# Kernel optimization log

Hardware: AMD Instinct MI355X
Metric: run time of the kernel (lower is better)

Reference implementation:

```python
import jax, jax.numpy as jnp
import numpy as np

B, N, NB, E, H, A, K, D = 32, 512, 10, 1024, 256, 82, 4, 3


def setup_inputs() -> dict:
    key = jax.random.key(0)
    ks = iter(jax.random.split(key, 64))
    f = lambda shape: jax.random.normal(next(ks), shape, jnp.float32) * 0.05
    inp = {
        "atom_fea": jax.random.normal(next(ks), (B, N, A), jnp.float32),
        "bond_fea": jax.random.normal(next(ks), (B, E, 6), jnp.float32),
        "d_anb": jax.random.randint(next(ks), (B, N, NB), 0, N),
        "d_bnb": jax.random.randint(next(ks), (B, N, NB), 0, E),
        "d_nbs_mask": (jax.random.uniform(next(ks), (B, N, NB)) < 0.8).astype(jnp.float32),
        "d_mask": (jax.random.uniform(next(ks), (B, N)) < 0.9).astype(jnp.float32),
        "Wv": f((A, H)), "bv": f((H,)),
        "Wa_main": f((D, K, H, H)), "ba_main": f((D, K, H)),
        "Wa_super": f((D, K, H, H)), "ba_super": f((D, K, H)),
        "Wm": f((D, K, H, H)), "bm": f((D, K, H)),
        "Wbmm": f((D, K, H)), "bbmm": f((D, K)),
        "Wm2s": f((D, K * H, H)), "bm2s": f((D, H)),
        "Ws2m": f((D, H, H)), "bs2m": f((D, H)),
        "Wsup": f((D, H, H)), "bsup": f((D, H)),
        "Wzm1": f((D, H, H)), "bzm1": f((D, H)),
        "Wzm2": f((D, H, H)), "bzm2": f((D, H)),
        "Wzs1": f((D, H, H)), "bzs1": f((D, H)),
        "Wzs2": f((D, H, H)), "bzs2": f((D, H)),
        "Wu2": f((D, H + 6, H)), "bu2": f((D, H)),
        "Wu1": f((D, 2 * H, H)), "bu1": f((D, H)),
    }
    return inp


def mask_softmax(a, mask):
    a_max = jnp.max(a, -1, keepdims=True)
    e = jnp.exp(a - a_max) * mask
    return e / (jnp.sum(e, -1, keepdims=True) + 1e-6)


def _forward(atom_fea, bond_fea, d_nbs_mask, d_mask,
             Wv, bv, Wa_main, ba_main, Wa_super, ba_super, Wm, bm, Wbmm, bbmm,
             Wm2s, bm2s, Ws2m, bs2m, Wsup, bsup,
             Wzm1, bzm1, Wzm2, bzm2, Wzs1, bzs1, Wzs2, bzs2,
             Wu2, bu2, Wu1, bu1, d_anb, d_bnb):
    Bn = atom_fea.shape[0]
    bidx = jnp.arange(Bn)[:, None, None]
    # vertex embedding (default leaky_relu slope 0.01)
    vf = jax.nn.leaky_relu(atom_fea @ Wv + bv, 0.01)            # [B,N,H]
    sf = jnp.sum(vf * d_mask[:, :, None], axis=1, keepdims=True)  # [B,1,H]
    mask3 = d_nbs_mask[..., None]                               # [B,N,NB,1]
    for d in range(D):
        # --- multi-head main->super attention (vectorized over heads k) ---
        a_main = jnp.tanh(jnp.einsum('bnh,khj->bknj', vf, Wa_main[d]) + ba_main[d][None, :, None, :])
        a_super = jnp.tanh(jnp.einsum('boh,khj->bkoj', sf, Wa_super[d]) + ba_super[d][None, :, None, :])
        a = jnp.einsum('bknh,kh->bkn', a_main * a_super, Wbmm[d]) + bbmm[d][None, :, None]
        attn = mask_softmax(a, d_mask[:, None, :])               # [B,K,N]
        mvf = jnp.einsum('bnh,khj->bknj', vf, Wm[d]) + bm[d][None, :, None, :]
        m2s = jnp.einsum('bkn,bknh->bkh', attn, mvf).reshape(Bn, 1, K * H)
        main_to_super = jnp.tanh(m2s @ Wm2s[d] + bm2s[d])        # [B,1,H]
        # --- wln unit: gather neighbors, MLP, masked sum (slope 0.1) ---
        vnei = vf[bidx, d_anb]                                   # [B,N,NB,H]
        enei = bond_fea[bidx, d_bnb]                             # [B,N,NB,6]
        lnei = jnp.concatenate([vnei, enei], -1)                 # [B,N,NB,H+6]
        nei = jax.nn.leaky_relu(lnei @ Wu2[d] + bu2[d], 0.1)
        nei = jnp.sum(nei * mask3, axis=2)                       # [B,N,H]
        main_self = jax.nn.leaky_relu(jnp.concatenate([vf, nei], -1) @ Wu1[d] + bu1[d], 0.1)
        # --- GRU-style gated updates ---
        super_to_main = jnp.tanh(sf @ Ws2m[d] + bs2m[d])         # [B,1,H]
        super_self = jnp.tanh(sf @ Wsup[d] + bsup[d])            # [B,1,H]
        z_main = jax.nn.sigmoid(main_self @ Wzm1[d] + bzm1[d] + super_to_main @ Wzm2[d] + bzm2[d])
        vf = (1 - z_main) * main_self + z_main * super_to_main
        z_sup = jax.nn.sigmoid(super_self @ Wzs1[d] + bzs1[d] + main_to_super @ Wzs2[d] + bzs2[d])
        sf = (1 - z_sup) * super_self + z_sup * main_to_super    # [B,1,H]; sum over dim 1 is a no-op
    return vf, sf


def reference(atom_fea, bond_fea, d_anb, d_bnb, d_nbs_mask, d_mask,
              Wv, bv, Wa_main, ba_main, Wa_super, ba_super, Wm, bm, Wbmm, bbmm,
              Wm2s, bm2s, Ws2m, bs2m, Wsup, bsup,
              Wzm1, bzm1, Wzm2, bzm2, Wzs1, bzs1, Wzs2, bzs2,
              Wu2, bu2, Wu1, bu1):
    return _forward(atom_fea, bond_fea, d_nbs_mask, d_mask,
                    Wv, bv, Wa_main, ba_main, Wa_super, ba_super, Wm, bm, Wbmm, bbmm,
                    Wm2s, bm2s, Ws2m, bs2m, Wsup, bsup,
                    Wzm1, bzm1, Wzm2, bzm2, Wzs1, bzs1, Wzs2, bzs2,
                    Wu2, bu2, Wu1, bu1, d_anb, d_bnb)
```

## Files before the change

### kernel.cpp

```cpp
#include <hip/hip_runtime.h>
#include <hip/hip_bf16.h>

#define B_ 32
#define N_ 512
#define NB_ 10
#define E_ 1024
#define H_ 256
#define A_ 82
#define K_ 4
#define D_ 3
#define M_ (B_*N_)

typedef unsigned short u16;
typedef __attribute__((ext_vector_type(8))) short bf16x8;
typedef __attribute__((ext_vector_type(4))) float f32x4;

__device__ __forceinline__ float b2f(u16 u){
    unsigned int x = ((unsigned int)u) << 16;
    return __builtin_bit_cast(float, x);
}
__device__ __forceinline__ u16 f2b(float f){
    unsigned int x = __builtin_bit_cast(unsigned int, f);
    unsigned int lsb = (x >> 16) & 1u;
    x += 0x7fffu + lsb;
    return (u16)(x >> 16);
}
__device__ __forceinline__ float sigmoidf_(float x){ return 1.f/(1.f+expf(-x)); }

static constexpr int CVT_N[31] = {
    B_*E_*6, B_*N_*NB_, B_*N_,
    A_*H_, H_,
    D_*K_*H_*H_, D_*K_*H_, D_*K_*H_*H_, D_*K_*H_,
    D_*K_*H_*H_, D_*K_*H_, D_*K_*H_, D_*K_,
    D_*K_*H_*H_, D_*H_, D_*H_*H_, D_*H_,
    D_*H_*H_, D_*H_, D_*H_*H_, D_*H_,
    D_*H_*H_, D_*H_, D_*H_*H_, D_*H_,
    D_*H_*H_, D_*H_, D_*(H_+6)*H_, D_*H_,
    D_*2*H_*H_, D_*H_
};
struct Offs { long v[32]; };
static constexpr Offs mk_offs(){
    Offs o{}; o.v[0]=0;
    for(int i=0;i<31;i++) o.v[i+1]=o.v[i]+CVT_N[i];
    return o;
}
static constexpr Offs CVT_OFF = mk_offs();

struct Ptrs { const void* p[31]; };

__global__ void k_detect(const unsigned short* __restrict__ wv_raw, int* __restrict__ flag){
    float v = b2f(wv_raw[threadIdx.x]);
    bool plaus = (v==v) && (fabsf(v) < 100.0f);
    unsigned long long m = __ballot(plaus);
    if (threadIdx.x==0) *flag = (m == ~0ULL) ? 1 : 0;
}

__global__ void k_cvt(Ptrs ptrs, float* __restrict__ dst, const int* __restrict__ flag){
    long i4 = (long)blockIdx.x*256 + threadIdx.x;
    const long TOT4 = CVT_OFF.v[31]/4;
    if (i4 >= TOT4) return;
    long e = i4*4;
    int t = 0;
    #pragma unroll
    for(int i=1;i<31;i++) t += (e >= CVT_OFF.v[i]) ? 1 : 0;
    long l4 = i4 - CVT_OFF.v[t]/4;
    const void* src = ptrs.p[t];
    float4 o;
    if (*flag){
        ushort4 u = ((const ushort4*)src)[l4];
        o.x=b2f(u.x); o.y=b2f(u.y); o.z=b2f(u.z); o.w=b2f(u.w);
    } else {
        o = ((const float4*)src)[l4];
    }
    *(float4*)(dst + CVT_OFF.v[t] + l4*4) = o;
}

__global__ void k_wt(const float* __restrict__ Wam, const float* __restrict__ Wu2,
                     const float* __restrict__ Wu1, const float* __restrict__ Wzm1,
                     u16* __restrict__ WT){
    int mi = blockIdx.z;
    const float* src;
    if (mi<12)      src = Wam  + (size_t)mi*H_*H_;
    else if (mi<15) src = Wu2  + (size_t)(mi-12)*(H_+6)*H_;
    else if (mi<18) src = Wu1  + (size_t)(mi-15)*2*H_*H_;
    else if (mi<21) src = Wu1  + (size_t)(mi-18)*2*H_*H_ + (size_t)H_*H_;
    else            src = Wzm1 + (size_t)(mi-21)*H_*H_;
    __shared__ float t[32][33];
    int x = threadIdx.x, y = threadIdx.y;
    int k0 = blockIdx.y*32, n0 = blockIdx.x*32;
    for(int yy=y; yy<32; yy+=8) t[yy][x] = src[(size_t)(k0+yy)*H_ + n0+x];
    __syncthreads();
    u16* dst = WT + ((size_t)mi*8 + (k0>>5))*8192;
    int quad = x>>3, j = x&7;
    for(int yy=y; yy<32; yy+=8){
        int n = n0+yy, nt = n>>4, lv = n&15;
        dst[nt*512 + quad*128 + lv*8 + j] = f2b(t[x][yy]);
    }
}

__global__ void k_embed(const u16* __restrict__ atom, const float* __restrict__ Wv,
                        const float* __restrict__ bv, float* __restrict__ vf,
                        u16* __restrict__ vf_bf, const int* __restrict__ flag){
    __shared__ float arow[8][A_];
    int r0 = blockIdx.x*8; int j = threadIdx.x;
    int fl = *flag;
    for(int i=j;i<8*A_;i+=256){
        int r=i/A_, a=i-r*A_;
        arow[r][a] = fl ? b2f(atom[(size_t)(r0+r)*A_+a])
                        : ((const float*)atom)[(size_t)(r0+r)*A_+a];
    }
    __syncthreads();
    float acc[8];
    float bj = bv[j];
    #pragma unroll
    for(int r=0;r<8;r++) acc[r]=bj;
    for(int a=0;a<A_;a++){
        float w = Wv[a*H_+j];
        #pragma unroll
        for(int r=0;r<8;r++) acc[r] += arow[r][a]*w;
    }
    #pragma unroll
    for(int r=0;r<8;r++){
        float v = acc[r];
        v = v>0.f ? v : 0.01f*v;
        vf[(size_t)(r0+r)*H_+j] = v;
        vf_bf[(size_t)(r0+r)*H_+j] = f2b(v);
    }
}

__global__ void k_sf0(const float* __restrict__ vf, const float* __restrict__ dmask,
                      float* __restrict__ sf){
    int b = blockIdx.x, h = threadIdx.x;
    __shared__ float mk[N_];
    for(int n=threadIdx.x;n<N_;n+=256) mk[n] = dmask[b*N_+n];
    __syncthreads();
    float s=0.f;
    #pragma unroll 8
    for(int n=0;n<N_;n++) s += mk[n]*vf[((size_t)b*N_+n)*H_ + h];
    sf[b*H_+h]=s;
}

__global__ void k_s1(int d, const float* __restrict__ sf,
    const float* __restrict__ Was, const float* __restrict__ bas,
    const float* __restrict__ Wbmm,
    const float* __restrict__ Ws2m, const float* __restrict__ bs2m,
    const float* __restrict__ Wsup, const float* __restrict__ bsup,
    const float* __restrict__ Wzm2, const float* __restrict__ bzm2,
    float* __restrict__ asw, float* __restrict__ s2m, float* __restrict__ ssf,
    float* __restrict__ st)
{
    int b = blockIdx.x, m = blockIdx.y, j = threadIdx.x;
    __shared__ float sfl[H_];
    __shared__ float s2l[H_];
    sfl[j] = sf[b*H_+j];
    __syncthreads();
    if (m == 6){
        const float* W = Ws2m + (size_t)d*H_*H_;
        float acc = bs2m[d*H_+j];
        #pragma unroll 8
        for(int h=0;h<H_;h++) acc += sfl[h]*W[h*H_+j];
        s2l[j] = tanhf(acc);
        __syncthreads();
        const float* W2 = Wzm2 + (size_t)d*H_*H_;
        float acc2 = bzm2[d*H_+j];
        #pragma unroll 8
        for(int h=0;h<H_;h++) acc2 += s2l[h]*W2[h*H_+j];
        st[b*H_+j] = acc2;
        return;
    }
    const float* W; float bias;
    if (m < 4){ W = Was + (size_t)(d*K_+m)*H_*H_; bias = bas[(d*K_+m)*H_+j]; }
    else if (m==4){ W = Ws2m + (size_t)d*H_*H_; bias = bs2m[d*H_+j]; }
    else { W = Wsup + (size_t)d*H_*H_; bias = bsup[d*H_+j]; }
    float acc = bias;
    #pragma unroll 8
    for(int h=0;h<H_;h++) acc += sfl[h]*W[h*H_+j];
    float v = tanhf(acc);
    if (m < 4) asw[(b*K_+m)*H_+j] = v * Wbmm[(d*K_+m)*H_+j];
    else if (m==4) s2m[b*H_+j] = v;
    else ssf[b*H_+j] = v;
}

__device__ __forceinline__ void stageW(const u16* __restrict__ g, u16* l){
    int t = threadIdx.x;
    const u16* gs = g + t*8;
    u16* ls = l + t*8;
    #pragma unroll
    for(int it=0; it<4; ++it)
        __builtin_amdgcn_global_load_lds(
            (const __attribute__((address_space(1))) void*)(gs + it*2048),
            (__attribute__((address_space(3))) void*)(ls + it*2048),
            16, 0, 0);
}

__device__ __forceinline__ void gemm_ldsW(const u16* __restrict__ Abf,
                                          const u16* __restrict__ WTg,
                                          u16* Wlds, f32x4 acc[2][8])
{
    int tid = threadIdx.x;
    int lane = tid & 63, wave = tid >> 6;
    int wy = wave >> 1, wx = wave & 1;
    int quad = lane >> 4, l15 = lane & 15;
    const u16* aP0 = Abf + (size_t)(wy*32 + l15)*H_ + quad*8;
    const u16* aP1 = aP0 + 16*H_;
    bf16x8 a[4][2];
    #pragma unroll
    for(int s=0;s<3;s++){
        a[s][0] = *(const bf16x8*)(aP0 + s*32);
        a[s][1] = *(const bf16x8*)(aP1 + s*32);
    }
    stageW(WTg, Wlds);
    #pragma unroll
    for(int mt=0;mt<2;mt++)
        #pragma unroll
        for(int nt=0;nt<8;nt++) acc[mt][nt]=(f32x4){0.f,0.f,0.f,0.f};
    __syncthreads();
    #pragma unroll
    for(int s=0;s<8;s++){
        if (s<7) stageW(WTg + (size_t)(s+1)*8192, Wlds + ((s+1)&1)*8192);
        if (s<5){
            int sl = s+3;
            a[sl&3][0] = *(const bf16x8*)(aP0 + sl*32);
            a[sl&3][1] = *(const bf16x8*)(aP1 + sl*32);
        }
        const u16* wb = Wlds + (s&1)*8192 + wx*4096 + quad*128 + l15*8;
        bf16x8 w[8];
        #pragma unroll
        for(int nt=0;nt<8;nt++) w[nt] = *(const bf16x8*)(wb + nt*512);
        #pragma unroll
        for(int mt=0;mt<2;mt++)
            #pragma unroll
            for(int nt=0;nt<8;nt++)
                acc[mt][nt] = __builtin_amdgcn_mfma_f32_16x16x32_bf16(
                    a[s&3][mt], w[nt], acc[mt][nt], 0,0,0);
        __syncthreads();
    }
}

__device__ __forceinline__ void gemm_lds2(const u16* Als, const u16* __restrict__ WTg,
                                          u16* Wlds, f32x4 acc[2][8])
{
    int tid = threadIdx.x;
    int lane = tid & 63, wave = tid >> 6;
    int wy = wave >> 1, wx = wave & 1;
    int quad = lane >> 4, l15 = lane & 15;
    stageW(WTg, Wlds);
    #pragma unroll
    for(int mt=0;mt<2;mt++)
        #pragma unroll
        for(int nt=0;nt<8;nt++) acc[mt][nt]=(f32x4){0.f,0.f,0.f,0.f};
    __syncthreads();
    int r0 = wy*32 + l15, r1 = r0 + 16;
    #pragma unroll
    for(int s=0;s<8;s++){
        if (s<7) stageW(WTg + (size_t)(s+1)*8192, Wlds + ((s+1)&1)*8192);
        int c0 = s*32 + quad*8;
        bf16x8 a0 = *(const bf16x8*)(Als + r0*256 + (c0 ^ ((r0&7)<<3)));
        bf16x8 a1 = *(const bf16x8*)(Als + r1*256 + (c0 ^ ((r1&7)<<3)));
        const u16* wb = Wlds + (s&1)*8192 + wx*4096 + quad*128 + l15*8;
        bf16x8 w[8];
        #pragma unroll
        for(int nt=0;nt<8;nt++) w[nt] = *(const bf16x8*)(wb + nt*512);
        #pragma unroll
        for(int nt=0;nt<8;nt++){
            acc[0][nt] = __builtin_amdgcn_mfma_f32_16x16x32_bf16(a0, w[nt], acc[0][nt], 0,0,0);
            acc[1][nt] = __builtin_amdgcn_mfma_f32_16x16x32_bf16(a1, w[nt], acc[1][nt], 0,0,0);
        }
        __syncthreads();
    }
}

__global__ __launch_bounds__(256,3) void k_gemm_big(int d, const u16* __restrict__ vf_bf,
    const u16* __restrict__ WT, const float* __restrict__ ba_main,
    const float* __restrict__ bbmm, const float* __restrict__ bu1,
    const float* __restrict__ asw, float* __restrict__ score,
    float* __restrict__ proj_u2, float* __restrict__ pu1a)
{
    __shared__ __attribute__((aligned(16))) u16 Wlds[2*8192];
    int m0 = blockIdx.x*64;
    int seg = blockIdx.y;
    int b = m0 >> 9;
    int mi;
    if (seg < 4)      mi = d*4+seg;
    else if (seg==4)  mi = 12+d;
    else              mi = 15+d;
    f32x4 acc[2][8];
    gemm_ldsW(vf_bf + (size_t)m0*H_, WT + (size_t)mi*H_*H_, Wlds, acc);
    int tid=threadIdx.x, lane=tid&63, wave=tid>>6;
    int wy=wave>>1, wx=wave&1, quad=lane>>4, l15=lane&15;
    if (seg < 4){
        float* sred = (float*)Wlds;
        const float* aswp = asw + (size_t)(b*K_+seg)*H_;
        const float* bap  = ba_main + (size_t)(d*K_+seg)*H_;
        float bbv[8], awv[8];
        #pragma unroll
        for(int nt=0;nt<8;nt++){
            int col = wx*128+nt*16+l15;
            bbv[nt]=bap[col]; awv[nt]=aswp[col];
        }
        #pragma unroll
        for(int mt=0;mt<2;mt++)
            #pragma unroll
            for(int r=0;r<4;r++){
                float p=0.f;
                #pragma unroll
                for(int nt=0;nt<8;nt++)
                    p += tanhf(acc[mt][nt][r]+bbv[nt])*awv[nt];
                int row = wy*32+mt*16+quad*4+r;
                sred[row*33 + wx*16+l15] = p;
            }
        __syncthreads();
        if (tid < 64){
            float s=0.f;
            #pragma unroll 8
            for(int i=0;i<32;i++) s += sred[tid*33+i];
            score[(size_t)(b*K_+seg)*N_ + (m0&511) + tid] = s + bbmm[d*K_+seg];
        }
    } else if (seg==4){
        #pragma unroll
        for(int mt=0;mt<2;mt++)
            #pragma unroll
            for(int nt=0;nt<8;nt++){
                int col = wx*128+nt*16+l15;
                #pragma unroll
                for(int r=0;r<4;r++){
                    int row = m0 + wy*32+mt*16+quad*4+r;
                    proj_u2[(size_t)row*H_+col] = acc[mt][nt][r];
                }
            }
    } else {
        const float* bp = bu1 + d*H_;
        #pragma unroll
        for(int mt=0;mt<2;mt++)
            #pragma unroll
            for(int nt=0;nt<8;nt++){
                int col = wx*128+nt*16+l15;
                float bb = bp[col];
                #pragma unroll
                for(int r=0;r<4;r++){
                    int row = m0 + wy*32+mt*16+quad*4+r;
                    pu1a[(size_t)row*H_+col] = acc[mt][nt][r] + bb;
                }
            }
    }
}

__global__ __launch_bounds__(256,2) void k_msup(int d, const u16* __restrict__ neims,
    const u16* __restrict__ WT, const float* __restrict__ pu1a,
    const float* __restrict__ bzm1, const float* __restrict__ st,
    const float* __restrict__ s2m, float* __restrict__ vf, u16* __restrict__ vf_bf)
{
    __shared__ __attribute__((aligned(16))) u16 Wlds[2*8192];
    __shared__ __attribute__((aligned(16))) u16 ms_lds[64*256];
    int m0 = blockIdx.x*64; int b = m0>>9;
    f32x4 acc[2][8];
    gemm_ldsW(neims + (size_t)m0*H_, WT + (size_t)(18+d)*H_*H_, Wlds, acc);
    int tid=threadIdx.x, lane=tid&63, wave=tid>>6;
    int wy=wave>>1, wx=wave&1, quad=lane>>4, l15=lane&15;
    #pragma unroll
    for(int mt=0;mt<2;mt++)
        #pragma unroll
        for(int nt=0;nt<8;nt++){
            int col = wx*128+nt*16+l15;
            #pragma unroll
            for(int r=0;r<4;r++){
                int rl = wy*32+mt*16+quad*4+r;
                float v = acc[mt][nt][r] + pu1a[(size_t)(m0+rl)*H_+col];
                v = v>0.f? v : 0.1f*v;
                acc[mt][nt][r] = v;
                ms_lds[rl*256 + (col ^ ((rl&7)<<3))] = f2b(v);
            }
        }
    f32x4 acc2[2][8];
    gemm_lds2(ms_lds, WT + (size_t)(21+d)*H_*H_, Wlds, acc2);
    #pragma unroll
    for(int mt=0;mt<2;mt++)
        #pragma unroll
        for(int nt=0;nt<8;nt++){
            int col = wx*128+nt*16+l15;
            float bz = bzm1[d*H_+col];
            float stv = st[b*H_+col];
            float sm = s2m[b*H_+col];
            #pragma unroll
            for(int r=0;r<4;r++){
                int row = m0 + wy*32+mt*16+quad*4+r;
                float z = sigmoidf_(acc2[mt][nt][r] + bz + stv);
                float msv = acc[mt][nt][r];
                float o = (1.f-z)*msv + z*sm;
                vf[(size_t)row*H_+col] = o;
                vf_bf[(size_t)row*H_+col] = f2b(o);
            }
        }
}

__global__ __launch_bounds__(512) void k_att(int d, const float* __restrict__ score,
    const float* __restrict__ dmask, const float* __restrict__ vf,
    const float* __restrict__ Wm, const float* __restrict__ bm,
    float* __restrict__ m2s)
{
    int b = blockIdx.x, k = blockIdx.y, tid = threadIdx.x;
    __shared__ float at[N_];
    __shared__ float sh[256];
    __shared__ float tp[2][256];
    const float* a = score + (size_t)(b*K_+k)*N_;
    float v0=0.f, v1=0.f, e0=0.f, e1=0.f;
    if (tid < 256){ v0=a[tid]; v1=a[tid+256]; sh[tid]=fmaxf(v0,v1); }
    __syncthreads();
    for(int s=128;s>0;s>>=1){ if(tid<s) sh[tid]=fmaxf(sh[tid],sh[tid+s]); __syncthreads(); }
    float m = sh[0]; __syncthreads();
    if (tid < 256){
        e0 = expf(v0-m)*dmask[b*N_+tid];
        e1 = expf(v1-m)*dmask[b*N_+tid+256];
        sh[tid]=e0+e1;
    }
    __syncthreads();
    for(int s=128;s>0;s>>=1){ if(tid<s) sh[tid]+=sh[tid+s]; __syncthreads(); }
    float S = sh[0];
    float inv = 1.f/(S+1e-6f);
    float sumattn = S*inv;
    if (tid < 256){ at[tid]=e0*inv; at[tid+256]=e1*inv; }
    __syncthreads();
    int h = tid & 255, half = tid >> 8;
    {
        float acc=0.f;
        const float* vfp = vf + ((size_t)b*N_ + half*256)*H_ + h;
        const float* atp = at + half*256;
        #pragma unroll 8
        for(int n=0;n<256;n++) acc += atp[n]*vfp[(size_t)n*H_];
        tp[half][h]=acc;
    }
    __syncthreads();
    {
        const float* W = Wm + (size_t)(d*K_+k)*H_*H_;
        float acc = (half==0) ? sumattn*bm[(d*K_+k)*H_+h] : 0.f;
        int h0 = half*128;
        #pragma unroll 8
        for(int t2=h0; t2<h0+128; t2++) acc += (tp[0][t2]+tp[1][t2])*W[(size_t)t2*H_+h];
        at[half*256+h]=acc;
    }
    __syncthreads();
    if (tid < 256) m2s[(size_t)(b*K_+k)*H_+tid] = at[tid]+at[256+tid];
}

__global__ void k_m2(int d, const float* __restrict__ m2s, const float* __restrict__ Wm2s,
                     float* __restrict__ mtsp)
{
    int b=blockIdx.x, c=blockIdx.y, j=threadIdx.x;
    __shared__ float xl[H_];
    xl[j]=m2s[(size_t)(b*K_+c)*H_+j];
    __syncthreads();
    const float* W = Wm2s + (size_t)d*(K_*H_)*H_ + (size_t)(c*H_)*H_;
    float acc=0.f;
    #pragma unroll 8
    for(int h=0;h<H_;h++) acc += xl[h]*W[h*H_+j];
    mtsp[((size_t)c*B_+b)*H_+j]=acc;
}

__global__ __launch_bounds__(512) void k_fin(int d, const float* __restrict__ mtsp,
    const float* __restrict__ bm2s, const float* __restrict__ ssf,
    const float* __restrict__ Wzs1, const float* __restrict__ Wzs2,
    const float* __restrict__ bzs1, const float* __restrict__ bzs2,
    float* __restrict__ sf)
{
    int b = blockIdx.x, tid = threadIdx.x;
    int j = tid & 255, g = tid >> 8;
    __shared__ float mtsl[256], ssl[256], pp[2][256];
    if (g==0){
        float acc = bm2s[d*H_+j];
        #pragma unroll
        for(int c=0;c<4;c++) acc += mtsp[((size_t)c*B_+b)*H_+j];
        mtsl[j] = tanhf(acc);
    } else {
        ssl[j] = ssf[b*H_+j];
    }
    __syncthreads();
    {
        const float* W = (g ? Wzs2 : Wzs1) + (size_t)d*H_*H_;
        const float* x = g ? mtsl : ssl;
        float acc = 0.f;
        #pragma unroll 8
        for(int h=0;h<H_;h++) acc += x[h]*W[h*H_+j];
        pp[g][j] = acc;
    }
    __syncthreads();
    if (g==0){
        float z = sigmoidf_(pp[0][j]+bzs1[d*H_+j]+pp[1][j]+bzs2[d*H_+j]);
        sf[b*H_+j] = (1.f-z)*ssl[j] + z*mtsl[j];
    }
}

__global__ void k_nei(int d, const int* __restrict__ anb, const int* __restrict__ bnb,
    const float* __restrict__ nbm, const float* __restrict__ bond,
    const float* __restrict__ Wu2, const float* __restrict__ bu2,
    const float* __restrict__ proj_u2, u16* __restrict__ nei_bf)
{
    __shared__ float W2s[6][256];
    __shared__ float bfeat[4][NB_][6];
    __shared__ int ai[4][NB_]; __shared__ int bi[4][NB_]; __shared__ float mk[4][NB_];
    int r0 = blockIdx.x*4; int b = r0 >> 9; int h = threadIdx.x;
    const float* W2 = Wu2 + (size_t)d*(H_+6)*H_ + (size_t)H_*H_;
    for(int i=h;i<6*H_;i+=256) W2s[i>>8][i&255] = W2[i];
    if (h < 4*NB_){
        int r=h/NB_, jn=h-r*NB_;
        ai[r][jn]=anb[(size_t)(r0+r)*NB_+jn];
        bi[r][jn]=bnb[(size_t)(r0+r)*NB_+jn];
        mk[r][jn]=nbm[(size_t)(r0+r)*NB_+jn];
    }
    __syncthreads();
    if (h < 4*NB_*6){
        int r=h/(NB_*6), rem=h-r*(NB_*6), jn=rem/6, i=rem-jn*6;
        bfeat[r][jn][i]=bond[((size_t)b*E_+bi[r][jn])*6+i];
    }
    __syncthreads();
    float bu = bu2[d*H_+h];
    #pragma unroll
    for(int r=0;r<4;r++){
        float acc=0.f;
        #pragma unroll
        for(int jn=0;jn<NB_;jn++){
            float v = proj_u2[((size_t)b*N_+ai[r][jn])*H_+h] + bu;
            #pragma unroll
            for(int i=0;i<6;i++) v += bfeat[r][jn][i]*W2s[i][h];
            v = v>0.f? v : 0.1f*v;
            acc += mk[r][jn]*v;
        }
        nei_bf[(size_t)(r0+r)*H_+h]=f2b(acc);
    }
}

__global__ void k_out(const float* __restrict__ vf, const float* __restrict__ sf,
                      void* __restrict__ out, const int* __restrict__ flag){
    int idx = blockIdx.x*256 + threadIdx.x;
    const int total = M_*H_ + B_*H_;
    if (idx >= total) return;
    float v = (idx < M_*H_) ? vf[idx] : sf[idx - M_*H_];
    if (*flag) ((unsigned short*)out)[idx] = f2b(v);
    else       ((float*)out)[idx] = v;
}

extern "C" void kernel_launch(void* const* d_in, const int* in_sizes, int n_in,
                              void* d_out, int out_size, void* d_ws, size_t ws_size,
                              hipStream_t stream)
{
    const int* anb = (const int*)d_in[2];
    const int* bnb = (const int*)d_in[3];

    float* ws   = (float*)d_ws;
    int*   flag = (int*)ws;
    float* cvt  = ws + 64;
    float* p    = cvt + ((CVT_OFF.v[31] + 63) & ~63L);
    float* vf        = p; p += (size_t)M_*H_;
    float* proj_u2   = p; p += (size_t)M_*H_;
    float* proj_u1a  = p; p += (size_t)M_*H_;
    u16*   vf_bf     = (u16*)p; p += (size_t)M_*H_/2;
    u16*   neims     = (u16*)p; p += (size_t)M_*H_/2;
    float* sf        = p; p += B_*H_;
    float* score     = p; p += B_*K_*N_;
    float* asw       = p; p += B_*K_*H_;
    float* s2m       = p; p += B_*H_;
    float* ssf       = p; p += B_*H_;
    float* st        = p; p += B_*H_;
    float* m2s       = p; p += B_*K_*H_;
    float* mtsp      = p; p += 4*B_*H_;
    u16*   WT        = (u16*)p;

    const float* cBond = cvt + CVT_OFF.v[0];
    const float* cNbm  = cvt + CVT_OFF.v[1];
    const float* cDm   = cvt + CVT_OFF.v[2];
    const float* cWv   = cvt + CVT_OFF.v[3];
    const float* cbv   = cvt + CVT_OFF.v[4];
    const float* cWam  = cvt + CVT_OFF.v[5];
    const float* cbam  = cvt + CVT_OFF.v[6];
    const float* cWas  = cvt + CVT_OFF.v[7];
    const float* cbas  = cvt + CVT_OFF.v[8];
    const float* cWm   = cvt + CVT_OFF.v[9];
    const float* cbm   = cvt + CVT_OFF.v[10];
    const float* cWbmm = cvt + CVT_OFF.v[11];
    const float* cbbmm = cvt + CVT_OFF.v[12];
    const float* cWm2s = cvt + CVT_OFF.v[13];
    const float* cbm2s = cvt + CVT_OFF.v[14];
    const float* cWs2m = cvt + CVT_OFF.v[15];
    const float* cbs2m = cvt + CVT_OFF.v[16];
    const float* cWsup = cvt + CVT_OFF.v[17];
    const float* cbsup = cvt + CVT_OFF.v[18];
    const float* cWzm1 = cvt + CVT_OFF.v[19];
    const float* cbzm1 = cvt + CVT_OFF.v[20];
    const float* cWzm2 = cvt + CVT_OFF.v[21];
    const float* cbzm2 = cvt + CVT_OFF.v[22];
    const float* cWzs1 = cvt + CVT_OFF.v[23];
    const float* cbzs1 = cvt + CVT_OFF.v[24];
    const float* cWzs2 = cvt + CVT_OFF.v[25];
    const float* cbzs2 = cvt + CVT_OFF.v[26];
    const float* cWu2  = cvt + CVT_OFF.v[27];
    const float* cbu2  = cvt + CVT_OFF.v[28];
    const float* cWu1  = cvt + CVT_OFF.v[29];
    const float* cbu1  = cvt + CVT_OFF.v[30];

    Ptrs ptrs;
    {
        int idx[31] = {1,4,5,6,7,8,9,10,11,12,13,14,15,16,17,18,19,20,21,
                       22,23,24,25,26,27,28,29,30,31,32,33};
        for(int i=0;i<31;i++) ptrs.p[i] = d_in[idx[i]];
    }

    k_detect<<<1,64,0,stream>>>((const unsigned short*)d_in[6], flag);
    {
        long tot4 = CVT_OFF.v[31]/4;
        int gx = (int)((tot4 + 255)/256);
        k_cvt<<<gx,256,0,stream>>>(ptrs, cvt, flag);
    }
    k_wt<<<dim3(8,8,24),dim3(32,8),0,stream>>>(cWam, cWu2, cWu1, cWzm1, WT);

    k_embed<<<M_/8,256,0,stream>>>((const u16*)d_in[0], cWv, cbv, vf, vf_bf, flag);
    k_sf0<<<B_,256,0,stream>>>(vf, cDm, sf);
    for(int d=0; d<D_; d++){
        k_s1<<<dim3(B_,7),256,0,stream>>>(d, sf, cWas, cbas, cWbmm,
                                          cWs2m, cbs2m, cWsup, cbsup,
                                          cWzm2, cbzm2, asw, s2m, ssf, st);
        k_gemm_big<<<dim3(M_/64,6),256,0,stream>>>(d, vf_bf, WT, cbam, cbbmm, cbu1,
                                                   asw, score, proj_u2, proj_u1a);
        k_att<<<dim3(B_,K_),512,0,stream>>>(d, score, cDm, vf, cWm, cbm, m2s);
        k_nei<<<M_/4,256,0,stream>>>(d, anb, bnb, cNbm, cBond, cWu2, cbu2, proj_u2, neims);
        k_msup<<<M_/64,256,0,stream>>>(d, neims, WT, proj_u1a, cbzm1, st, s2m, vf, vf_bf);
        k_m2<<<dim3(B_,4),256,0,stream>>>(d, m2s, cWm2s, mtsp);
        k_fin<<<B_,512,0,stream>>>(d, mtsp, cbm2s, ssf, cWzs1, cWzs2, cbzs1, cbzs2, sf);
    }
    k_out<<<(M_*H_+B_*H_+255)/256,256,0,stream>>>(vf, sf, d_out, flag);
}
```

Before: 651.6 us.

## Fuse neighbor aggregation into msup GEMM and enlarge big-GEMM row tile

```diff
diff --git a/kernel.cpp b/kernel.cpp
--- a/kernel.cpp
+++ b/kernel.cpp
@@ -193,46 +193,46 @@
             16, 0, 0);
 }
 
-__device__ __forceinline__ void gemm_ldsW(const u16* __restrict__ Abf,
-                                          const u16* __restrict__ WTg,
-                                          u16* Wlds, f32x4 acc[2][8])
+__device__ __forceinline__ void gemm_ldsW128(const u16* __restrict__ Abf,
+                                             const u16* __restrict__ WTg,
+                                             u16* Wlds, f32x4 acc[4][8])
 {
     int tid = threadIdx.x;
     int lane = tid & 63, wave = tid >> 6;
     int wy = wave >> 1, wx = wave & 1;
     int quad = lane >> 4, l15 = lane & 15;
-    const u16* aP0 = Abf + (size_t)(wy*32 + l15)*H_ + quad*8;
-    const u16* aP1 = aP0 + 16*H_;
-    bf16x8 a[4][2];
-    #pragma unroll
-    for(int s=0;s<3;s++){
-        a[s][0] = *(const bf16x8*)(aP0 + s*32);
-        a[s][1] = *(const bf16x8*)(aP1 + s*32);
-    }
+    const u16* aP = Abf + (size_t)(wy*64 + l15)*H_ + quad*8;
+    bf16x8 aA[4], aB[4];
+    #pragma unroll
+    for(int mt=0;mt<4;mt++) aA[mt] = *(const bf16x8*)(aP + (size_t)mt*16*H_);
     stageW(WTg, Wlds);
     #pragma unroll
-    for(int mt=0;mt<2;mt++)
+    for(int mt=0;mt<4;mt++)
         #pragma unroll
         for(int nt=0;nt<8;nt++) acc[mt][nt]=(f32x4){0.f,0.f,0.f,0.f};
     __syncthreads();
     #pragma unroll
     for(int s=0;s<8;s++){
-        if (s<7) stageW(WTg + (size_t)(s+1)*8192, Wlds + ((s+1)&1)*8192);
-        if (s<5){
-            int sl = s+3;
-            a[sl&3][0] = *(const bf16x8*)(aP0 + sl*32);
-            a[sl&3][1] = *(const bf16x8*)(aP1 + sl*32);
+        if (s<7){
+            stageW(WTg + (size_t)(s+1)*8192, Wlds + ((s+1)&1)*8192);
+            #pragma unroll
+            for(int mt=0;mt<4;mt++){
+                bf16x8 t = *(const bf16x8*)(aP + (s+1)*32 + (size_t)mt*16*H_);
+                if (s&1) aA[mt] = t; else aB[mt] = t;
+            }
         }
         const u16* wb = Wlds + (s&1)*8192 + wx*4096 + quad*128 + l15*8;
         bf16x8 w[8];
         #pragma unroll
         for(int nt=0;nt<8;nt++) w[nt] = *(const bf16x8*)(wb + nt*512);
         #pragma unroll
-        for(int mt=0;mt<2;mt++)
+        for(int mt=0;mt<4;mt++){
+            bf16x8 av = (s&1) ? aB[mt] : aA[mt];
             #pragma unroll
             for(int nt=0;nt<8;nt++)
                 acc[mt][nt] = __builtin_amdgcn_mfma_f32_16x16x32_bf16(
-                    a[s&3][mt], w[nt], acc[mt][nt], 0,0,0);
+                    av, w[nt], acc[mt][nt], 0,0,0);
+        }
         __syncthreads();
     }
 }
@@ -270,22 +270,22 @@
     }
 }
 
-__global__ __launch_bounds__(256,3) void k_gemm_big(int d, const u16* __restrict__ vf_bf,
+__global__ __launch_bounds__(256,2) void k_gemm_big(int d, const u16* __restrict__ vf_bf,
     const u16* __restrict__ WT, const float* __restrict__ ba_main,
     const float* __restrict__ bbmm, const float* __restrict__ bu1,
     const float* __restrict__ asw, float* __restrict__ score,
     float* __restrict__ proj_u2, float* __restrict__ pu1a)
 {
     __shared__ __attribute__((aligned(16))) u16 Wlds[2*8192];
-    int m0 = blockIdx.x*64;
+    int m0 = blockIdx.x*128;
     int seg = blockIdx.y;
     int b = m0 >> 9;
     int mi;
     if (seg < 4)      mi = d*4+seg;
     else if (seg==4)  mi = 12+d;
     else              mi = 15+d;
-    f32x4 acc[2][8];
-    gemm_ldsW(vf_bf + (size_t)m0*H_, WT + (size_t)mi*H_*H_, Wlds, acc);
+    f32x4 acc[4][8];
+    gemm_ldsW128(vf_bf + (size_t)m0*H_, WT + (size_t)mi*H_*H_, Wlds, acc);
     int tid=threadIdx.x, lane=tid&63, wave=tid>>6;
     int wy=wave>>1, wx=wave&1, quad=lane>>4, l15=lane&15;
     if (seg < 4){
@@ -299,18 +299,18 @@
             bbv[nt]=bap[col]; awv[nt]=aswp[col];
         }
         #pragma unroll
-        for(int mt=0;mt<2;mt++)
+        for(int mt=0;mt<4;mt++)
             #pragma unroll
             for(int r=0;r<4;r++){
                 float p=0.f;
                 #pragma unroll
                 for(int nt=0;nt<8;nt++)
                     p += tanhf(acc[mt][nt][r]+bbv[nt])*awv[nt];
-                int row = wy*32+mt*16+quad*4+r;
+                int row = wy*64+mt*16+quad*4+r;
                 sred[row*33 + wx*16+l15] = p;
             }
         __syncthreads();
-        if (tid < 64){
+        if (tid < 128){
             float s=0.f;
             #pragma unroll 8
             for(int i=0;i<32;i++) s += sred[tid*33+i];
@@ -318,44 +318,86 @@
         }
     } else if (seg==4){
         #pragma unroll
-        for(int mt=0;mt<2;mt++)
+        for(int mt=0;mt<4;mt++)
             #pragma unroll
             for(int nt=0;nt<8;nt++){
                 int col = wx*128+nt*16+l15;
                 #pragma unroll
                 for(int r=0;r<4;r++){
-                    int row = m0 + wy*32+mt*16+quad*4+r;
+                    int row = m0 + wy*64+mt*16+quad*4+r;
                     proj_u2[(size_t)row*H_+col] = acc[mt][nt][r];
                 }
             }
     } else {
         const float* bp = bu1 + d*H_;
         #pragma unroll
-        for(int mt=0;mt<2;mt++)
+        for(int mt=0;mt<4;mt++)
             #pragma unroll
             for(int nt=0;nt<8;nt++){
                 int col = wx*128+nt*16+l15;
                 float bb = bp[col];
                 #pragma unroll
                 for(int r=0;r<4;r++){
-                    int row = m0 + wy*32+mt*16+quad*4+r;
+                    int row = m0 + wy*64+mt*16+quad*4+r;
                     pu1a[(size_t)row*H_+col] = acc[mt][nt][r] + bb;
                 }
             }
     }
 }
 
-__global__ __launch_bounds__(256,2) void k_msup(int d, const u16* __restrict__ neims,
-    const u16* __restrict__ WT, const float* __restrict__ pu1a,
-    const float* __restrict__ bzm1, const float* __restrict__ st,
-    const float* __restrict__ s2m, float* __restrict__ vf, u16* __restrict__ vf_bf)
+__global__ __launch_bounds__(256,2) void k_neimsup(int d,
+    const int* __restrict__ anb, const int* __restrict__ bnb,
+    const float* __restrict__ nbm, const float* __restrict__ bond,
+    const float* __restrict__ Wu2, const float* __restrict__ bu2,
+    const float* __restrict__ proj_u2, const u16* __restrict__ WT,
+    const float* __restrict__ pu1a, const float* __restrict__ bzm1,
+    const float* __restrict__ st, const float* __restrict__ s2m,
+    float* __restrict__ vf, u16* __restrict__ vf_bf)
 {
     __shared__ __attribute__((aligned(16))) u16 Wlds[2*8192];
-    __shared__ __attribute__((aligned(16))) u16 ms_lds[64*256];
+    __shared__ __attribute__((aligned(16))) u16 tile[64*256];
+    __shared__ int   ai_s[64][NB_];
+    __shared__ int   bi_s[64][NB_];
+    __shared__ float mk_s[64][NB_];
     int m0 = blockIdx.x*64; int b = m0>>9;
+    int tid = threadIdx.x;
+    for(int i=tid;i<64*NB_;i+=256){
+        int r=i/NB_, jn=i-r*NB_;
+        ai_s[r][jn]=anb[(size_t)(m0+r)*NB_+jn];
+        bi_s[r][jn]=bnb[(size_t)(m0+r)*NB_+jn];
+        mk_s[r][jn]=nbm[(size_t)(m0+r)*NB_+jn];
+    }
+    __syncthreads();
+    float* bfs = (float*)Wlds;
+    for(int i=tid;i<64*NB_*6;i+=256){
+        int r=i/(NB_*6), rem=i-r*(NB_*6), jn=rem/6, ii=rem-jn*6;
+        bfs[i]=bond[((size_t)b*E_+bi_s[r][jn])*6+ii];
+    }
+    __syncthreads();
+    {
+        int h = tid;
+        const float* W2 = Wu2 + (size_t)d*(H_+6)*H_ + (size_t)H_*H_;
+        float bu = bu2[d*H_+h];
+        float w2r[6];
+        #pragma unroll
+        for(int i=0;i<6;i++) w2r[i]=W2[(size_t)i*H_+h];
+        for(int r=0;r<64;r++){
+            float acc=0.f;
+            #pragma unroll
+            for(int jn=0;jn<NB_;jn++){
+                float v = proj_u2[((size_t)b*N_+ai_s[r][jn])*H_+h] + bu;
+                #pragma unroll
+                for(int i=0;i<6;i++) v += bfs[(r*NB_+jn)*6+i]*w2r[i];
+                v = v>0.f? v : 0.1f*v;
+                acc += mk_s[r][jn]*v;
+            }
+            tile[r*256 + (h ^ ((r&7)<<3))] = f2b(acc);
+        }
+    }
+    __syncthreads();
     f32x4 acc[2][8];
-    gemm_ldsW(neims + (size_t)m0*H_, WT + (size_t)(18+d)*H_*H_, Wlds, acc);
-    int tid=threadIdx.x, lane=tid&63, wave=tid>>6;
+    gemm_lds2(tile, WT + (size_t)(18+d)*H_*H_, Wlds, acc);
+    int lane=tid&63, wave=tid>>6;
     int wy=wave>>1, wx=wave&1, quad=lane>>4, l15=lane&15;
     #pragma unroll
     for(int mt=0;mt<2;mt++)
@@ -368,11 +410,11 @@
                 float v = acc[mt][nt][r] + pu1a[(size_t)(m0+rl)*H_+col];
                 v = v>0.f? v : 0.1f*v;
                 acc[mt][nt][r] = v;
-                ms_lds[rl*256 + (col ^ ((rl&7)<<3))] = f2b(v);
+                tile[rl*256 + (col ^ ((rl&7)<<3))] = f2b(v);
             }
         }
     f32x4 acc2[2][8];
-    gemm_lds2(ms_lds, WT + (size_t)(21+d)*H_*H_, Wlds, acc2);
+    gemm_lds2(tile, WT + (size_t)(21+d)*H_*H_, Wlds, acc2);
     #pragma unroll
     for(int mt=0;mt<2;mt++)
         #pragma unroll
@@ -489,45 +531,6 @@
     }
 }
 
-__global__ void k_nei(int d, const int* __restrict__ anb, const int* __restrict__ bnb,
-    const float* __restrict__ nbm, const float* __restrict__ bond,
-    const float* __restrict__ Wu2, const float* __restrict__ bu2,
-    const float* __restrict__ proj_u2, u16* __restrict__ nei_bf)
-{
-    __shared__ float W2s[6][256];
-    __shared__ float bfeat[4][NB_][6];
-    __shared__ int ai[4][NB_]; __shared__ int bi[4][NB_]; __shared__ float mk[4][NB_];
-    int r0 = blockIdx.x*4; int b = r0 >> 9; int h = threadIdx.x;
-    const float* W2 = Wu2 + (size_t)d*(H_+6)*H_ + (size_t)H_*H_;
-    for(int i=h;i<6*H_;i+=256) W2s[i>>8][i&255] = W2[i];
-    if (h < 4*NB_){
-        int r=h/NB_, jn=h-r*NB_;
-        ai[r][jn]=anb[(size_t)(r0+r)*NB_+jn];
-        bi[r][jn]=bnb[(size_t)(r0+r)*NB_+jn];
-        mk[r][jn]=nbm[(size_t)(r0+r)*NB_+jn];
-    }
-    __syncthreads();
-    if (h < 4*NB_*6){
-        int r=h/(NB_*6), rem=h-r*(NB_*6), jn=rem/6, i=rem-jn*6;
-        bfeat[r][jn][i]=bond[((size_t)b*E_+bi[r][jn])*6+i];
-    }
-    __syncthreads();
-    float bu = bu2[d*H_+h];
-    #pragma unroll
-    for(int r=0;r<4;r++){
-        float acc=0.f;
-        #pragma unroll
-        for(int jn=0;jn<NB_;jn++){
-            float v = proj_u2[((size_t)b*N_+ai[r][jn])*H_+h] + bu;
-            #pragma unroll
-            for(int i=0;i<6;i++) v += bfeat[r][jn][i]*W2s[i][h];
-            v = v>0.f? v : 0.1f*v;
-            acc += mk[r][jn]*v;
-        }
-        nei_bf[(size_t)(r0+r)*H_+h]=f2b(acc);
-    }
-}
-
 __global__ void k_out(const float* __restrict__ vf, const float* __restrict__ sf,
                       void* __restrict__ out, const int* __restrict__ flag){
     int idx = blockIdx.x*256 + threadIdx.x;
@@ -551,9 +554,8 @@
     float* p    = cvt + ((CVT_OFF.v[31] + 63) & ~63L);
     float* vf        = p; p += (size_t)M_*H_;
     float* proj_u2   = p; p += (size_t)M_*H_;
-    float* proj_u1a  = p; p += (size_t)M_*H_;
+    float* pu1a      = p; p += (size_t)M_*H_;
     u16*   vf_bf     = (u16*)p; p += (size_t)M_*H_/2;
-    u16*   neims     = (u16*)p; p += (size_t)M_*H_/2;
     float* sf        = p; p += B_*H_;
     float* score     = p; p += B_*K_*N_;
     float* asw       = p; p += B_*K_*H_;
@@ -617,11 +619,11 @@
         k_s1<<<dim3(B_,7),256,0,stream>>>(d, sf, cWas, cbas, cWbmm,
                                           cWs2m, cbs2m, cWsup, cbsup,
                                           cWzm2, cbzm2, asw, s2m, ssf, st);
-        k_gemm_big<<<dim3(M_/64,6),256,0,stream>>>(d, vf_bf, WT, cbam, cbbmm, cbu1,
-                                                   asw, score, proj_u2, proj_u1a);
+        k_gemm_big<<<dim3(M_/128,6),256,0,stream>>>(d, vf_bf, WT, cbam, cbbmm, cbu1,
+                                                    asw, score, proj_u2, pu1a);
         k_att<<<dim3(B_,K_),512,0,stream>>>(d, score, cDm, vf, cWm, cbm, m2s);
-        k_nei<<<M_/4,256,0,stream>>>(d, anb, bnb, cNbm, cBond, cWu2, cbu2, proj_u2, neims);
-        k_msup<<<M_/64,256,0,stream>>>(d, neims, WT, proj_u1a, cbzm1, st, s2m, vf, vf_bf);
+        k_neimsup<<<M_/64,256,0,stream>>>(d, anb, bnb, cNbm, cBond, cWu2, cbu2,
+                                          proj_u2, WT, pu1a, cbzm1, st, s2m, vf, vf_bf);
         k_m2<<<dim3(B_,4),256,0,stream>>>(d, m2s, cWm2s, mtsp);
         k_fin<<<B_,512,0,stream>>>(d, mtsp, cbm2s, ssf, cWzs1, cWzs2, cbzs1, cbzs2, sf);
     }
```

Result: slower. 711.6 us (+9.2%).
